# Performance work log

Measured on AMD Instinct MI355X. Metric: run time of the kernel, lower is better.

## Reference

```python
import jax, jax.numpy as jnp
import numpy as np

B = 64          # batch == number of parallel fc layers used
T = 512         # sequence length
IN_FEATS = 1024
OUT_FEATS = 1024


def setup_inputs() -> dict:
    key = jax.random.key(0)
    kx, kw, kb = jax.random.split(key, 3)
    x = jax.random.normal(kx, (B, T, IN_FEATS), dtype=jnp.float32)
    # Per-sample Linear weights, stacked: W[i] is the weight of list_fc[i]
    # (torch Linear weight layout: [out_feats, in_feats])
    bound = 1.0 / np.sqrt(IN_FEATS)
    W = jax.random.uniform(kw, (B, OUT_FEATS, IN_FEATS), dtype=jnp.float32,
                           minval=-bound, maxval=bound)
    b = jax.random.uniform(kb, (B, OUT_FEATS), dtype=jnp.float32,
                           minval=-bound, maxval=bound)
    return {"x": x, "W": W, "b": b}


def reference(x, W, b):
    # Equivalent to: cat([list_fc[i](x[i:i+1]) for i in range(B)], dim=0)
    # i.e. a grouped GEMM with group size 1: out[i] = x[i] @ W[i].T + b[i]
    out = jnp.einsum('bti,boi->bto', x, W)  # [B, T, OUT]
    return out + b[:, None, :]
```

## Files before the change

### kernel.cpp

```cpp
#include <hip/hip_runtime.h>
#include <hip/hip_bf16.h>

#define BATCH 64
#define MDIM 512
#define NDIM 1024
#define KDIM 1024

#define BM 256
#define BN 256
#define BK 64
#define NKT (KDIM / BK)

typedef __attribute__((ext_vector_type(4))) float f32x4;
typedef __attribute__((ext_vector_type(8))) short bf16x8;
typedef __attribute__((ext_vector_type(4))) unsigned int u32x4;

__device__ __forceinline__ unsigned int cvt2(float lo, float hi) {
    __hip_bfloat162 h = __float22bfloat162_rn(float2{lo, hi});
    return *(unsigned int*)&h;
}

#define MFMA16(a, b, c) __builtin_amdgcn_mfma_f32_16x16x32_bf16((a), (b), (c), 0, 0, 0)

#define PHASE_MID do { __builtin_amdgcn_sched_barrier(0); \
    __builtin_amdgcn_s_barrier(); \
    asm volatile("s_waitcnt lgkmcnt(0)" ::: "memory"); \
    __builtin_amdgcn_sched_barrier(0); \
    __builtin_amdgcn_s_setprio(1); } while (0)
#define PHASE_END do { __builtin_amdgcn_s_setprio(0); \
    __builtin_amdgcn_sched_barrier(0); \
    __builtin_amdgcn_s_barrier(); \
    __builtin_amdgcn_sched_barrier(0); } while (0)

__global__ __launch_bounds__(512, 2)
void grouped_fc_kernel(const float* __restrict__ X,
                       const float* __restrict__ W,
                       const float* __restrict__ Bias,
                       float* __restrict__ Out) {
    const int swz  = (blockIdx.x & 7) * 64 + (blockIdx.x >> 3);
    const int bidx = swz >> 3;
    const int tile = swz & 7;
    const int tm = tile & 1;
    const int tn = tile >> 1;

    const int tid  = threadIdx.x;
    const int lane = tid & 63;
    const int wid  = tid >> 6;
    const int wm   = wid & 1;
    const int wn   = wid >> 1;

    __shared__ unsigned short ldsA[2][BM][BK];
    __shared__ unsigned short ldsB[2][BN][BK];

    const float* srcA = X + ((size_t)bidx * MDIM + (size_t)tm * BM) * KDIM;
    const float* srcB = W + ((size_t)bidx * NDIM + (size_t)tn * BN) * KDIM;

    const int s_r  = tid >> 2;
    const int s_cf = (tid & 3) * 16;
    const int s_x  = s_r & 7;
    const int so0  = (((tid & 3) * 2)     ^ s_x) * 8;
    const int so1  = (((tid & 3) * 2 + 1) ^ s_x) * 8;

    f32x4 st0[4], st1[4];

    auto ISSUE = [&](const float* srcbase, int hv, int kt_, f32x4 (&s)[4]) {
        const float* p = srcbase + (size_t)(hv * 128 + s_r) * KDIM + kt_ * BK + s_cf;
#pragma unroll
        for (int v = 0; v < 4; ++v) s[v] = *(const f32x4*)(p + v * 4);
    };

    auto CVTW = [&](unsigned short* ldsbase, int hv, f32x4 (&s)[4]) {
        const int row = hv * 128 + s_r;
        u32x4 w0, w1;
        w0[0] = cvt2(s[0][0], s[0][1]); w0[1] = cvt2(s[0][2], s[0][3]);
        w0[2] = cvt2(s[1][0], s[1][1]); w0[3] = cvt2(s[1][2], s[1][3]);
        w1[0] = cvt2(s[2][0], s[2][1]); w1[1] = cvt2(s[2][2], s[2][3]);
        w1[2] = cvt2(s[3][0], s[3][1]); w1[3] = cvt2(s[3][2], s[3][3]);
        *(u32x4*)&ldsbase[(size_t)row * BK + so0] = w0;
        *(u32x4*)&ldsbase[(size_t)row * BK + so1] = w1;
    };

    const int frow = lane & 15;
    const int khi  = lane >> 4;
    const int xr   = frow & 7;
    const int oK0  = ((khi)     ^ xr) * 8;
    const int oK1  = ((4 + khi) ^ xr) * 8;

    f32x4 acc[8][4];
#pragma unroll
    for (int mi = 0; mi < 8; ++mi)
#pragma unroll
        for (int ni = 0; ni < 4; ++ni)
            acc[mi][ni] = (f32x4){0.f, 0.f, 0.f, 0.f};

    ISSUE(srcA, 0, 0, st0); ISSUE(srcA, 1, 0, st1);
    CVTW(&ldsA[0][0][0], 0, st0); CVTW(&ldsA[0][0][0], 1, st1);
    ISSUE(srcB, 0, 0, st0); ISSUE(srcB, 1, 0, st1);
    CVTW(&ldsB[0][0][0], 0, st0); CVTW(&ldsB[0][0][0], 1, st1);
    ISSUE(srcA, 0, 1, st0); ISSUE(srcA, 1, 1, st1);
    asm volatile("s_waitcnt lgkmcnt(0)" ::: "memory");
    __builtin_amdgcn_sched_barrier(0);
    __builtin_amdgcn_s_barrier();
    __builtin_amdgcn_sched_barrier(0);

#pragma unroll 1
    for (int kt = 0; kt < NKT; ++kt) {
        const int cur = kt & 1;
        const bool m1 = (kt + 1 < NKT);
        const bool m2 = (kt + 2 < NKT);
        unsigned short* nA = &ldsA[cur ^ 1][0][0];
        unsigned short* nB = &ldsB[cur ^ 1][0][0];
        bf16x8 af[8], bfr[2];

#pragma unroll
        for (int mi = 0; mi < 8; ++mi)
            af[mi] = *(const bf16x8*)&ldsA[cur][wm * 128 + mi * 16 + frow][oK0];
        bfr[0] = *(const bf16x8*)&ldsB[cur][wn * 64 + 0 * 16 + frow][oK0];
        bfr[1] = *(const bf16x8*)&ldsB[cur][wn * 64 + 1 * 16 + frow][oK0];
        if (m1) { CVTW(nA, 0, st0); ISSUE(srcB, 0, kt + 1, st0); }
        PHASE_MID;
#pragma unroll
        for (int mi = 0; mi < 8; ++mi) {
            acc[mi][0] = MFMA16(af[mi], bfr[0], acc[mi][0]);
            acc[mi][1] = MFMA16(af[mi], bfr[1], acc[mi][1]);
        }
        PHASE_END;

        bfr[0] = *(const bf16x8*)&ldsB[cur][wn * 64 + 2 * 16 + frow][oK0];
        bfr[1] = *(const bf16x8*)&ldsB[cur][wn * 64 + 3 * 16 + frow][oK0];
        if (m1) { CVTW(nA, 1, st1); ISSUE(srcB, 1, kt + 1, st1); }
        PHASE_MID;
#pragma unroll
        for (int mi = 0; mi < 8; ++mi) {
            acc[mi][2] = MFMA16(af[mi], bfr[0], acc[mi][2]);
            acc[mi][3] = MFMA16(af[mi], bfr[1], acc[mi][3]);
        }
        PHASE_END;

#pragma unroll
        for (int mi = 0; mi < 8; ++mi)
            af[mi] = *(const bf16x8*)&ldsA[cur][wm * 128 + mi * 16 + frow][oK1];
        bfr[0] = *(const bf16x8*)&ldsB[cur][wn * 64 + 0 * 16 + frow][oK1];
        bfr[1] = *(const bf16x8*)&ldsB[cur][wn * 64 + 1 * 16 + frow][oK1];
        if (m1) CVTW(nB, 0, st0);
        if (m2) ISSUE(srcA, 0, kt + 2, st0);
        PHASE_MID;
#pragma unroll
        for (int mi = 0; mi < 8; ++mi) {
            acc[mi][0] = MFMA16(af[mi], bfr[0], acc[mi][0]);
            acc[mi][1] = MFMA16(af[mi], bfr[1], acc[mi][1]);
        }
        PHASE_END;

        bfr[0] = *(const bf16x8*)&ldsB[cur][wn * 64 + 2 * 16 + frow][oK1];
        bfr[1] = *(const bf16x8*)&ldsB[cur][wn * 64 + 3 * 16 + frow][oK1];
        if (m1) CVTW(nB, 1, st1);
        if (m2) ISSUE(srcA, 1, kt + 2, st1);
        PHASE_MID;
#pragma unroll
        for (int mi = 0; mi < 8; ++mi) {
            acc[mi][2] = MFMA16(af[mi], bfr[0], acc[mi][2]);
            acc[mi][3] = MFMA16(af[mi], bfr[1], acc[mi][3]);
        }
        PHASE_END;
    }

#pragma unroll
    for (int ni = 0; ni < 4; ++ni) {
        const int gc = tn * BN + wn * 64 + ni * 16 + frow;
        const float bv = Bias[bidx * NDIM + gc];
#pragma unroll
        for (int mi = 0; mi < 8; ++mi) {
            const int gr0 = tm * BM + wm * 128 + mi * 16 + (lane >> 4) * 4;
            float* po = Out + ((size_t)bidx * MDIM + gr0) * NDIM + gc;
#pragma unroll
            for (int r = 0; r < 4; ++r)
                po[(size_t)r * NDIM] = acc[mi][ni][r] + bv;
        }
    }
}

extern "C" void kernel_launch(void* const* d_in, const int* in_sizes, int n_in,
                              void* d_out, int out_size, void* d_ws, size_t ws_size,
                              hipStream_t stream) {
    const float* X  = (const float*)d_in[0];
    const float* W  = (const float*)d_in[1];
    const float* Bs = (const float*)d_in[2];
    float* Out = (float*)d_out;

    grouped_fc_kernel<<<dim3(512), dim3(512), 0, stream>>>(X, W, Bs, Out);
}
```

Baseline: 142.9 us.

## Replace four-phase barrier schedule with one barrier per K tile

Restructures the main loop from four barrier-separated phases per K tile to two half-K MFMA bursts with a single workgroup barrier at the end of each tile. Global loads for the next tile's A are issued at the top of the iteration, so the prefetch depth drops from two tiles ahead to one. The A conversion and B issue happen between the two compute halves, and the B conversion happens after the second. This cuts barrier count and setprio toggling, and it lets each wave run 32 MFMAs back-to-back. The cost is less latency hiding for global loads and less explicit interleaving of memory work with compute across waves.

```diff
diff --git a/kernel.cpp b/kernel.cpp
--- a/kernel.cpp
+++ b/kernel.cpp
@@ -22,12 +22,8 @@
 
 #define MFMA16(a, b, c) __builtin_amdgcn_mfma_f32_16x16x32_bf16((a), (b), (c), 0, 0, 0)
 
-#define PHASE_MID do { __builtin_amdgcn_sched_barrier(0); \
-    __builtin_amdgcn_s_barrier(); \
+#define TILE_SEAL do { \
     asm volatile("s_waitcnt lgkmcnt(0)" ::: "memory"); \
-    __builtin_amdgcn_sched_barrier(0); \
-    __builtin_amdgcn_s_setprio(1); } while (0)
-#define PHASE_END do { __builtin_amdgcn_s_setprio(0); \
     __builtin_amdgcn_sched_barrier(0); \
     __builtin_amdgcn_s_barrier(); \
     __builtin_amdgcn_sched_barrier(0); } while (0)
@@ -97,72 +93,56 @@
     CVTW(&ldsA[0][0][0], 0, st0); CVTW(&ldsA[0][0][0], 1, st1);
     ISSUE(srcB, 0, 0, st0); ISSUE(srcB, 1, 0, st1);
     CVTW(&ldsB[0][0][0], 0, st0); CVTW(&ldsB[0][0][0], 1, st1);
-    ISSUE(srcA, 0, 1, st0); ISSUE(srcA, 1, 1, st1);
-    asm volatile("s_waitcnt lgkmcnt(0)" ::: "memory");
-    __builtin_amdgcn_sched_barrier(0);
-    __builtin_amdgcn_s_barrier();
-    __builtin_amdgcn_sched_barrier(0);
+    TILE_SEAL;
 
 #pragma unroll 1
     for (int kt = 0; kt < NKT; ++kt) {
-        const int cur = kt & 1;
+        const int rd = kt & 1;
         const bool m1 = (kt + 1 < NKT);
-        const bool m2 = (kt + 2 < NKT);
-        unsigned short* nA = &ldsA[cur ^ 1][0][0];
-        unsigned short* nB = &ldsB[cur ^ 1][0][0];
-        bf16x8 af[8], bfr[2];
+        unsigned short* nA = &ldsA[rd ^ 1][0][0];
+        unsigned short* nB = &ldsB[rd ^ 1][0][0];
+        bf16x8 af[8], bfr[4];
+
+        if (m1) { ISSUE(srcA, 0, kt + 1, st0); ISSUE(srcA, 1, kt + 1, st1); }
 
 #pragma unroll
         for (int mi = 0; mi < 8; ++mi)
-            af[mi] = *(const bf16x8*)&ldsA[cur][wm * 128 + mi * 16 + frow][oK0];
-        bfr[0] = *(const bf16x8*)&ldsB[cur][wn * 64 + 0 * 16 + frow][oK0];
-        bfr[1] = *(const bf16x8*)&ldsB[cur][wn * 64 + 1 * 16 + frow][oK0];
-        if (m1) { CVTW(nA, 0, st0); ISSUE(srcB, 0, kt + 1, st0); }
-        PHASE_MID;
+            af[mi] = *(const bf16x8*)&ldsA[rd][wm * 128 + mi * 16 + frow][oK0];
 #pragma unroll
-        for (int mi = 0; mi < 8; ++mi) {
-            acc[mi][0] = MFMA16(af[mi], bfr[0], acc[mi][0]);
-            acc[mi][1] = MFMA16(af[mi], bfr[1], acc[mi][1]);
+        for (int ni = 0; ni < 4; ++ni)
+            bfr[ni] = *(const bf16x8*)&ldsB[rd][wn * 64 + ni * 16 + frow][oK0];
+
+        __builtin_amdgcn_s_setprio(1);
+#pragma unroll
+        for (int mi = 0; mi < 8; ++mi)
+#pragma unroll
+            for (int ni = 0; ni < 4; ++ni)
+                acc[mi][ni] = MFMA16(af[mi], bfr[ni], acc[mi][ni]);
+        __builtin_amdgcn_s_setprio(0);
+
+        if (m1) {
+            CVTW(nA, 0, st0); CVTW(nA, 1, st1);
+            ISSUE(srcB, 0, kt + 1, st0); ISSUE(srcB, 1, kt + 1, st1);
         }
-        PHASE_END;
-
-        bfr[0] = *(const bf16x8*)&ldsB[cur][wn * 64 + 2 * 16 + frow][oK0];
-        bfr[1] = *(const bf16x8*)&ldsB[cur][wn * 64 + 3 * 16 + frow][oK0];
-        if (m1) { CVTW(nA, 1, st1); ISSUE(srcB, 1, kt + 1, st1); }
-        PHASE_MID;
-#pragma unroll
-        for (int mi = 0; mi < 8; ++mi) {
-            acc[mi][2] = MFMA16(af[mi], bfr[0], acc[mi][2]);
-            acc[mi][3] = MFMA16(af[mi], bfr[1], acc[mi][3]);
-        }
-        PHASE_END;
 
 #pragma unroll
         for (int mi = 0; mi < 8; ++mi)
-            af[mi] = *(const bf16x8*)&ldsA[cur][wm * 128 + mi * 16 + frow][oK1];
-        bfr[0] = *(const bf16x8*)&ldsB[cur][wn * 64 + 0 * 16 + frow][oK1];
-        bfr[1] = *(const bf16x8*)&ldsB[cur][wn * 64 + 1 * 16 + frow][oK1];
-        if (m1) CVTW(nB, 0, st0);
-        if (m2) ISSUE(srcA, 0, kt + 2, st0);
-        PHASE_MID;
+            af[mi] = *(const bf16x8*)&ldsA[rd][wm * 128 + mi * 16 + frow][oK1];
 #pragma unroll
-        for (int mi = 0; mi < 8; ++mi) {
-            acc[mi][0] = MFMA16(af[mi], bfr[0], acc[mi][0]);
-            acc[mi][1] = MFMA16(af[mi], bfr[1], acc[mi][1]);
-        }
-        PHASE_END;
+        for (int ni = 0; ni < 4; ++ni)
+            bfr[ni] = *(const bf16x8*)&ldsB[rd][wn * 64 + ni * 16 + frow][oK1];
 
-        bfr[0] = *(const bf16x8*)&ldsB[cur][wn * 64 + 2 * 16 + frow][oK1];
-        bfr[1] = *(const bf16x8*)&ldsB[cur][wn * 64 + 3 * 16 + frow][oK1];
-        if (m1) CVTW(nB, 1, st1);
-        if (m2) ISSUE(srcA, 1, kt + 2, st1);
-        PHASE_MID;
+        __builtin_amdgcn_s_setprio(1);
 #pragma unroll
-        for (int mi = 0; mi < 8; ++mi) {
-            acc[mi][2] = MFMA16(af[mi], bfr[0], acc[mi][2]);
-            acc[mi][3] = MFMA16(af[mi], bfr[1], acc[mi][3]);
-        }
-        PHASE_END;
+        for (int mi = 0; mi < 8; ++mi)
+#pragma unroll
+            for (int ni = 0; ni < 4; ++ni)
+                acc[mi][ni] = MFMA16(af[mi], bfr[ni], acc[mi][ni]);
+        __builtin_amdgcn_s_setprio(0);
+
+        if (m1) { CVTW(nB, 0, st0); CVTW(nB, 1, st1); }
+
+        TILE_SEAL;
     }
 
 #pragma unroll
```

After: 150.0 us. 1.05x slower.
